# Performance work log

Hardware: AMD Instinct MI355X
Metric: run time of the kernel (lower is better)

## Reference

```python
import jax, jax.numpy as jnp
import numpy as np

D_MODEL = 256
NHEAD = 8
HEAD_DIM = D_MODEL // NHEAD
EPS = 1e-6
LN_EPS = 1e-5


def embed_rotary(x, cos, sin):
    # x, cos, sin: [N, L, C]; rotate even/odd pairs (Lepard-style RoFPE)
    x2 = jnp.stack([-x[..., 1::2], x[..., ::2]], axis=-1).reshape(x.shape)
    return x * cos + x2 * sin


def layer_norm(x, g, b):
    m = jnp.mean(x, axis=-1, keepdims=True)
    v = jnp.mean((x - m) ** 2, axis=-1, keepdims=True)
    return (x - m) / jnp.sqrt(v + LN_EPS) * g + b


def setup_inputs() -> dict:
    key = jax.random.key(0)
    ks = jax.random.split(key, 12)
    N, L, S, C = 8, 4096, 4096, D_MODEL
    s = 1.0 / np.sqrt(C)
    return {
        "x": jax.random.normal(ks[0], (N, L, C), jnp.float32),
        "source": jax.random.normal(ks[1], (N, S, C), jnp.float32),
        "x_pe": jax.random.normal(ks[2], (N, L, C, 2), jnp.float32),
        "source_pe": jax.random.normal(ks[3], (N, S, C, 2), jnp.float32),
        "Wq": jax.random.normal(ks[4], (C, C), jnp.float32) * s,
        "Wk": jax.random.normal(ks[5], (C, C), jnp.float32) * s,
        "Wv": jax.random.normal(ks[6], (C, C), jnp.float32) * s,
        "Wm": jax.random.normal(ks[7], (C, C), jnp.float32) * s,
        "W1": jax.random.normal(ks[8], (2 * C, 2 * C), jnp.float32) * s,
        "W2": jax.random.normal(ks[9], (2 * C, C), jnp.float32) * s,
        "ln1_g": jnp.ones((C,), jnp.float32),
        "ln1_b": jnp.zeros((C,), jnp.float32),
        "ln2_g": jnp.ones((C,), jnp.float32),
        "ln2_b": jnp.zeros((C,), jnp.float32),
    }


def reference(x, source, x_pe, source_pe, Wq, Wk, Wv, Wm, W1, W2, ln1_g, ln1_b, ln2_g, ln2_b):
    N, L, C = x.shape
    S = source.shape[1]
    H, D = NHEAD, HEAD_DIM

    query = x @ Wq           # [N, L, C]
    key = source @ Wk        # [N, S, C]
    value = source @ Wv      # [N, S, C]

    # ELU+1 feature maps (on pre-rotary projections)
    Q = jax.nn.elu(query) + 1.0
    K = jax.nn.elu(key) + 1.0

    q_cos, q_sin = x_pe[..., 0], x_pe[..., 1]
    k_cos, k_sin = source_pe[..., 0], source_pe[..., 1]
    Q_pos = embed_rotary(query, q_cos, q_sin)
    K_pos = embed_rotary(key, k_cos, k_sin)
    value = embed_rotary(value, k_cos, k_sin)

    Q = Q.reshape(N, L, H, D)
    K = K.reshape(N, S, H, D)
    Q_pos = Q_pos.reshape(N, L, H, D)
    K_pos = K_pos.reshape(N, S, H, D)
    value = value.reshape(N, S, H, D)

    values = value / S
    KV = jnp.einsum('nshd,nshv->nhdv', K_pos, values)          # [N, H, D, D]
    Z = 1.0 / (jnp.einsum('nlhd,nhd->nlh', Q, K.sum(axis=1)) + EPS)
    queried = jnp.einsum('nlhd,nhdv->nlhv', Q_pos, KV) * Z[..., None] * S  # [N, L, H, D]

    message = queried.reshape(N, L, C) @ Wm
    message = layer_norm(message, ln1_g, ln1_b)
    h = jnp.concatenate([x, message], axis=2) @ W1             # [N, L, 2C]
    h = jax.nn.relu(h)
    message = h @ W2                                            # [N, L, C]
    message = layer_norm(message, ln2_g, ln2_b)
    return x + message
```

## Files before the change

kernel.cpp:

```cpp
#include <hip/hip_runtime.h>

typedef __attribute__((ext_vector_type(8))) short bf16x8;
typedef __attribute__((ext_vector_type(4))) float f32x4;

__device__ __forceinline__ float bf2f(unsigned short b) {
    unsigned u = ((unsigned)b) << 16; float f;
    __builtin_memcpy(&f, &u, 4); return f;
}
__device__ __forceinline__ unsigned short f2bf(float f) {
    unsigned u; __builtin_memcpy(&u, &f, 4);
    unsigned r = u + 0x7FFFu + ((u >> 16) & 1u);
    return (unsigned short)(r >> 16);
}
__device__ __forceinline__ unsigned packbf(float a, float b) {
    return (unsigned)f2bf(a) | ((unsigned)f2bf(b) << 16);
}
__device__ __forceinline__ float elu1(float v) { return v > 0.f ? v + 1.f : __expf(v); }

__device__ __forceinline__ void async_copy16(const unsigned short* g, unsigned short* l) {
    __builtin_amdgcn_global_load_lds(
        (const __attribute__((address_space(1))) unsigned int*)g,
        (__attribute__((address_space(3))) unsigned int*)l, 16, 0, 0);
}

__device__ __host__ __forceinline__ int chan_of(int tc) {
    return (tc & ~63) | ((tc & 15) << 1) | ((tc >> 4) & 1) | (((tc >> 5) & 1) << 5);
}
__device__ __forceinline__ int chan_even(int gnb, int p, int low) {
    const int tc = gnb + 32 * p + low;
    return (tc & ~63) | ((tc & 15) << 1) | (((tc >> 5) & 1) << 5);
}

#define EPI_RELU 0
#define EPI_Q 1
#define EPI_KV 2
#define EPI_LN1 3
#define EPI_LN2RES 4

template <int MT, int NT, int EPI>
__global__ __launch_bounds__(256) void gemm_bt(
    const unsigned short* __restrict__ A, int lda,
    const unsigned short* __restrict__ B, int K,
    unsigned short* __restrict__ Cb, int ldc,
    const float* __restrict__ pe,
    const float* __restrict__ KsumC, float* __restrict__ KsumA,
    float* __restrict__ Zbuf, unsigned short* __restrict__ Qpos,
    unsigned short* __restrict__ KF, unsigned short* __restrict__ VF,
    const float* __restrict__ g, const float* __restrict__ bta,
    unsigned short* __restrict__ A2out,
    const float* __restrict__ xres, float* __restrict__ outF)
{
    constexpr int WM = MT / 2, WN = NT / 2, MI = WM / 16, NI = WN / 16;
    __shared__ unsigned short Asm[MT * 32];
    __shared__ unsigned short Bsm[NT * 32];
    const int t = threadIdx.x;
    const int lane = t & 63, w = t >> 6;
    const int wm = w & 1, wn = w >> 1;
    const int quad = lane >> 4, low = lane & 15;
    const int m0 = blockIdx.x * MT, n0 = blockIdx.y * NT;

    f32x4 acc[MI][NI];
#pragma unroll
    for (int i = 0; i < MI; i++)
#pragma unroll
        for (int j = 0; j < NI; j++) acc[i][j] = (f32x4){0.f, 0.f, 0.f, 0.f};

    for (int k0 = 0; k0 < K; k0 += 32) {
        __syncthreads();
#pragma unroll
        for (int i = 0; i < MT / 64; i++) {
            const int chunk = i * 256 + t;
            const int row = chunk >> 2, part = chunk & 3;
            async_copy16(A + (size_t)(m0 + row) * lda + k0 + part * 8,
                         Asm + (i * 256 + w * 64) * 8);
        }
#pragma unroll
        for (int i = 0; i < NT / 64; i++) {
            const int chunk = i * 256 + t;
            const int row = chunk >> 2, part = chunk & 3;
            async_copy16(B + (size_t)(n0 + row) * K + k0 + part * 8,
                         Bsm + (i * 256 + w * 64) * 8);
        }
        __syncthreads();
        bf16x8 a[MI], b[NI];
#pragma unroll
        for (int mi = 0; mi < MI; mi++)
            a[mi] = *(const bf16x8*)&Asm[(wm * WM + mi * 16 + low) * 32 + quad * 8];
#pragma unroll
        for (int ni = 0; ni < NI; ni++)
            b[ni] = *(const bf16x8*)&Bsm[(wn * WN + ni * 16 + low) * 32 + quad * 8];
#pragma unroll
        for (int mi = 0; mi < MI; mi++)
#pragma unroll
            for (int ni = 0; ni < NI; ni++)
                acc[mi][ni] = __builtin_amdgcn_mfma_f32_16x16x32_bf16(a[mi], b[ni], acc[mi][ni], 0, 0, 0);
    }

    const int gmb = m0 + wm * WM, gnb = n0 + wn * WN;

    if constexpr (EPI == EPI_RELU) {
#pragma unroll
        for (int mi = 0; mi < MI; mi++)
#pragma unroll
            for (int p = 0; p < NI / 2; p++) {
                const int c_e = chan_even(gnb, p, low);
#pragma unroll
                for (int r = 0; r < 4; r++) {
                    const int row = gmb + mi * 16 + quad * 4 + r;
                    const float ve = acc[mi][2 * p][r], vo = acc[mi][2 * p + 1][r];
                    *(unsigned*)&Cb[(size_t)row * ldc + c_e] =
                        packbf(ve > 0.f ? ve : 0.f, vo > 0.f ? vo : 0.f);
                }
            }
    } else if constexpr (EPI == EPI_Q) {
        const int n = m0 >> 12;
#pragma unroll
        for (int p = 0; p < NI / 2; p++) {
            const int c_e = chan_even(gnb, p, low);
            const int head = c_e >> 5;
            const float2 ks = *(const float2*)&KsumC[n * 256 + c_e];
#pragma unroll
            for (int mi = 0; mi < MI; mi++) {
#pragma unroll
                for (int r = 0; r < 4; r++) {
                    const int row = gmb + mi * 16 + quad * 4 + r;
                    const float4 cs = *(const float4*)&pe[((size_t)row * 256 + c_e) * 2];
                    const float ve = acc[mi][2 * p][r], vo = acc[mi][2 * p + 1][r];
                    *(unsigned*)&Qpos[(size_t)row * 256 + c_e] =
                        packbf(ve * cs.x - vo * cs.y, vo * cs.z + ve * cs.w);
                    float z = elu1(ve) * ks.x + elu1(vo) * ks.y;
                    z += __shfl_xor(z, 1); z += __shfl_xor(z, 2);
                    z += __shfl_xor(z, 4); z += __shfl_xor(z, 8);
                    if (low == 0) Zbuf[(size_t)row * 8 + head] = 1.f / (z + 1e-6f);
                }
            }
        }
    } else if constexpr (EPI == EPI_KV) {
        const int n = m0 >> 12;
#pragma unroll
        for (int p = 0; p < NI / 2; p++) {
            const int c_full = chan_even(gnb, p, low);
            const bool isK = c_full < 256;
            const int c = c_full & 255;
            const int nh = n * 8 + (c >> 5), d = c & 31;
            unsigned short* dst = isK ? KF : VF;
            float kel_e = 0.f, kel_o = 0.f;
#pragma unroll
            for (int mi = 0; mi < MI; mi++) {
                const int row0 = gmb + mi * 16 + quad * 4;
                const int s0 = row0 & 4095;
                unsigned short pk[8];
#pragma unroll
                for (int r = 0; r < 4; r++) {
                    const int row = row0 + r;
                    const float4 cs = *(const float4*)&pe[((size_t)row * 256 + c) * 2];
                    const float ve = acc[mi][2 * p][r], vo = acc[mi][2 * p + 1][r];
                    pk[r]     = f2bf(ve * cs.x - vo * cs.y);
                    pk[4 + r] = f2bf(vo * cs.z + ve * cs.w);
                    if (isK) { kel_e += elu1(ve); kel_o += elu1(vo); }
                }
                const size_t base = ((size_t)nh * 512 + (s0 >> 3)) * 32;
                *(uint2*)&dst[(base + d) * 8 + (s0 & 7)]     = *(const uint2*)&pk[0];
                *(uint2*)&dst[(base + d + 1) * 8 + (s0 & 7)] = *(const uint2*)&pk[4];
            }
            if (isK) {
                kel_e += __shfl_xor(kel_e, 16); kel_e += __shfl_xor(kel_e, 32);
                kel_o += __shfl_xor(kel_o, 16); kel_o += __shfl_xor(kel_o, 32);
                if (quad == 0) {
                    atomicAdd(&KsumA[n * 256 + c], kel_e);
                    atomicAdd(&KsumA[n * 256 + c + 1], kel_o);
                }
            }
        }
    } else {
        __shared__ float2 lnp[2][64];
        __syncthreads();
#pragma unroll
        for (int mi = 0; mi < MI; mi++)
#pragma unroll
            for (int r = 0; r < 4; r++) {
                float s1 = 0.f, s2 = 0.f;
#pragma unroll
                for (int ni = 0; ni < NI; ni++) {
                    const float v = acc[mi][ni][r];
                    s1 += v; s2 += v * v;
                }
                s1 += __shfl_xor(s1, 1); s2 += __shfl_xor(s2, 1);
                s1 += __shfl_xor(s1, 2); s2 += __shfl_xor(s2, 2);
                s1 += __shfl_xor(s1, 4); s2 += __shfl_xor(s2, 4);
                s1 += __shfl_xor(s1, 8); s2 += __shfl_xor(s2, 8);
                if (low == 0) lnp[wn][wm * WM + mi * 16 + quad * 4 + r] = make_float2(s1, s2);
            }
        __syncthreads();
#pragma unroll
        for (int mi = 0; mi < MI; mi++)
#pragma unroll
            for (int r = 0; r < 4; r++) {
                const int rl = wm * WM + mi * 16 + quad * 4 + r;
                const int row = m0 + rl;
                const float2 pa = lnp[0][rl], pb = lnp[1][rl];
                const float mean = (pa.x + pb.x) * (1.f / 256.f);
                const float var = (pa.y + pb.y) * (1.f / 256.f) - mean * mean;
                const float rstd = rsqrtf(var + 1e-5f);
#pragma unroll
                for (int p = 0; p < NI / 2; p++) {
                    const int c_e = chan_even(gnb, p, low);
                    const float2 gg = *(const float2*)&g[c_e];
                    const float2 bb = *(const float2*)&bta[c_e];
                    const float ve = acc[mi][2 * p][r], vo = acc[mi][2 * p + 1][r];
                    const float oe = (ve - mean) * rstd * gg.x + bb.x;
                    const float oo = (vo - mean) * rstd * gg.y + bb.y;
                    if constexpr (EPI == EPI_LN1) {
                        *(unsigned*)&A2out[(size_t)row * 512 + 256 + c_e] = packbf(oe, oo);
                    } else {
                        const float2 xv = *(const float2*)&xres[(size_t)row * 256 + c_e];
                        float2 o; o.x = xv.x + oe; o.y = xv.y + oo;
                        *(float2*)&outF[(size_t)row * 256 + c_e] = o;
                    }
                }
            }
    }
}

__global__ void prep_weights(const float* __restrict__ Wq, const float* __restrict__ Wk,
                             const float* __restrict__ Wv, const float* __restrict__ Wm,
                             const float* __restrict__ W1, const float* __restrict__ W2,
                             unsigned short* __restrict__ WqT, unsigned short* __restrict__ WkvT,
                             unsigned short* __restrict__ WmT, unsigned short* __restrict__ W1T,
                             unsigned short* __restrict__ W2T, float* __restrict__ zero_base) {
    const int idx = blockIdx.x * 256 + threadIdx.x;
    if (idx < 65536) {
        const int tc = idx >> 8, k = idx & 255;
        WqT[idx] = f2bf(Wq[(size_t)k * 256 + chan_of(tc)]);
    } else if (idx < 196608) {
        const int i = idx - 65536, tc = i >> 8, k = i & 255;
        const int c = chan_of(tc);
        WkvT[i] = f2bf(c < 256 ? Wk[(size_t)k * 256 + c] : Wv[(size_t)k * 256 + (c - 256)]);
    } else if (idx < 262144) {
        const int i = idx - 196608, tc = i >> 8, k = i & 255;
        WmT[i] = f2bf(Wm[(size_t)k * 256 + chan_of(tc)]);
    } else if (idx < 524288) {
        const int i = idx - 262144, tc = i >> 9, k = i & 511;
        W1T[i] = f2bf(W1[(size_t)k * 512 + chan_of(tc)]);
    } else if (idx < 655360) {
        const int i = idx - 524288, tc = i >> 9, k = i & 511;
        W2T[i] = f2bf(W2[(size_t)k * 256 + chan_of(tc)]);
    } else {
        zero_base[idx - 655360] = 0.f;
    }
}

__global__ void conv_bf16(const float* __restrict__ src, unsigned short* __restrict__ dst, int dstride) {
    const int idx = blockIdx.x * 256 + threadIdx.x;
    const int row = idx >> 6;
    const int c0 = (idx & 63) * 4;
    const float4 v = *(const float4*)&src[(size_t)row * 256 + c0];
    unsigned short o[4] = {f2bf(v.x), f2bf(v.y), f2bf(v.z), f2bf(v.w)};
    *(uint2*)&dst[(size_t)row * dstride + c0] = *(const uint2*)o;
}

__global__ __launch_bounds__(256) void kv2_kernel(const unsigned short* __restrict__ KF,
                                                  const unsigned short* __restrict__ VF,
                                                  float* __restrict__ KVT) {
    const int nh = blockIdx.x, sc = blockIdx.y;
    const int t = threadIdx.x, lane = t & 63, w = t >> 6;
    const int quad = lane >> 4, low = lane & 15;
    const int sbase = sc * 1024 + w * 256;

    f32x4 acc[2][2];
#pragma unroll
    for (int i = 0; i < 2; i++)
#pragma unroll
        for (int j = 0; j < 2; j++) acc[i][j] = (f32x4){0.f, 0.f, 0.f, 0.f};

    for (int s0 = 0; s0 < 256; s0 += 32) {
        const int sk = sbase + s0 + quad * 8;
        const size_t cb = ((size_t)nh * 512 + (sk >> 3)) * 32;
        bf16x8 a[2], b[2];
#pragma unroll
        for (int mi = 0; mi < 2; mi++)
            a[mi] = *(const bf16x8*)&KF[(cb + mi * 16 + low) * 8];
#pragma unroll
        for (int ni = 0; ni < 2; ni++)
            b[ni] = *(const bf16x8*)&VF[(cb + ni * 16 + low) * 8];
#pragma unroll
        for (int mi = 0; mi < 2; mi++)
#pragma unroll
            for (int ni = 0; ni < 2; ni++)
                acc[mi][ni] = __builtin_amdgcn_mfma_f32_16x16x32_bf16(a[mi], b[ni], acc[mi][ni], 0, 0, 0);
    }

    __shared__ float red[4][1024];
#pragma unroll
    for (int mi = 0; mi < 2; mi++)
#pragma unroll
        for (int ni = 0; ni < 2; ni++)
#pragma unroll
            for (int r = 0; r < 4; r++)
                red[w][(mi * 16 + quad * 4 + r) * 32 + ni * 16 + low] = acc[mi][ni][r];
    __syncthreads();
#pragma unroll
    for (int k = 0; k < 4; k++) {
        const int i = t + k * 256;
        const float s = red[0][i] + red[1][i] + red[2][i] + red[3][i];
        atomicAdd(&KVT[(size_t)nh * 1024 + (size_t)(i & 31) * 32 + (i >> 5)], s);
    }
}

__global__ __launch_bounds__(256) void attn_out_kernel(const unsigned short* __restrict__ Qpos,
                                                       const float* __restrict__ KVT,
                                                       const float* __restrict__ Zbuf,
                                                       unsigned short* __restrict__ Qrd) {
    const int h = blockIdx.y, mt = blockIdx.x;
    const int t = threadIdx.x, lane = t & 63, w = t >> 6;
    const int quad = lane >> 4, low = lane & 15;
    const int rbase = mt * 256 + w * 64;
    const int n = rbase >> 12;

    bf16x8 b[2];
#pragma unroll
    for (int ni = 0; ni < 2; ni++) {
        const float* src = &KVT[((size_t)(n * 8 + h) * 32 + ni * 16 + low) * 32 + quad * 8];
        short tmp[8];
#pragma unroll
        for (int j = 0; j < 8; j++) tmp[j] = (short)f2bf(src[j]);
        __builtin_memcpy(&b[ni], tmp, 16);
    }

    f32x4 acc[4][2];
#pragma unroll
    for (int i = 0; i < 4; i++)
#pragma unroll
        for (int j = 0; j < 2; j++) acc[i][j] = (f32x4){0.f, 0.f, 0.f, 0.f};

#pragma unroll
    for (int mi = 0; mi < 4; mi++) {
        const bf16x8 a = *(const bf16x8*)&Qpos[((size_t)(rbase + mi * 16 + low)) * 256 + h * 32 + quad * 8];
#pragma unroll
        for (int ni = 0; ni < 2; ni++)
            acc[mi][ni] = __builtin_amdgcn_mfma_f32_16x16x32_bf16(a, b[ni], acc[mi][ni], 0, 0, 0);
    }

#pragma unroll
    for (int mi = 0; mi < 4; mi++)
#pragma unroll
        for (int ni = 0; ni < 2; ni++)
#pragma unroll
            for (int r = 0; r < 4; r++) {
                const int row = rbase + mi * 16 + quad * 4 + r;
                const int col = h * 32 + ni * 16 + low;
                Qrd[(size_t)row * 256 + col] = f2bf(acc[mi][ni][r] * Zbuf[(size_t)row * 8 + h]);
            }
}

extern "C" void kernel_launch(void* const* d_in, const int* in_sizes, int n_in,
                              void* d_out, int out_size, void* d_ws, size_t ws_size,
                              hipStream_t stream) {
    const float* x   = (const float*)d_in[0];
    const float* src = (const float*)d_in[1];
    const float* xpe = (const float*)d_in[2];
    const float* spe = (const float*)d_in[3];
    const float* Wq  = (const float*)d_in[4];
    const float* Wk  = (const float*)d_in[5];
    const float* Wv  = (const float*)d_in[6];
    const float* Wm  = (const float*)d_in[7];
    const float* W1  = (const float*)d_in[8];
    const float* W2  = (const float*)d_in[9];
    const float* g1  = (const float*)d_in[10];
    const float* b1  = (const float*)d_in[11];
    const float* g2  = (const float*)d_in[12];
    const float* b2  = (const float*)d_in[13];

    char* p = (char*)d_ws;
    unsigned short* WqT  = (unsigned short*)p; p += 256 * 256 * 2;
    unsigned short* WkvT = (unsigned short*)p; p += 512 * 256 * 2;
    unsigned short* WmT  = (unsigned short*)p; p += 256 * 256 * 2;
    unsigned short* W1T  = (unsigned short*)p; p += 512 * 512 * 2;
    unsigned short* W2T  = (unsigned short*)p; p += 256 * 512 * 2;
    float* KVT  = (float*)p; p += 64 * 1024 * 4;
    float* Ksum = (float*)p; p += 8 * 256 * 4;
    float* Zbuf = (float*)p; p += (size_t)32768 * 8 * 4;
    unsigned short* A2   = (unsigned short*)p; p += (size_t)32768 * 512 * 2;
    unsigned short* srcB = (unsigned short*)p; p += (size_t)32768 * 256 * 2;
    unsigned short* KF   = (unsigned short*)p; p += (size_t)32768 * 256 * 2;
    unsigned short* VF   = (unsigned short*)p; p += (size_t)32768 * 256 * 2;
    unsigned short* Qpos = (unsigned short*)p; p += (size_t)32768 * 256 * 2;
    unsigned short* Qrd  = (unsigned short*)p; p += (size_t)32768 * 256 * 2;
    unsigned short* hbuf = KF;

    prep_weights<<<2824, 256, 0, stream>>>(Wq, Wk, Wv, Wm, W1, W2,
                                           WqT, WkvT, WmT, W1T, W2T, KVT);
    conv_bf16<<<8192, 256, 0, stream>>>(x, A2, 512);
    conv_bf16<<<8192, 256, 0, stream>>>(src, srcB, 256);

    gemm_bt<128, 128, EPI_KV><<<dim3(256, 4), 256, 0, stream>>>(
        srcB, 256, WkvT, 256, nullptr, 0, spe, nullptr, Ksum,
        nullptr, nullptr, KF, VF, nullptr, nullptr, nullptr, nullptr, nullptr);
    kv2_kernel<<<dim3(64, 4), 256, 0, stream>>>(KF, VF, KVT);

    gemm_bt<128, 128, EPI_Q><<<dim3(256, 2), 256, 0, stream>>>(
        A2, 512, WqT, 256, nullptr, 0, xpe, Ksum, nullptr,
        Zbuf, Qpos, nullptr, nullptr, nullptr, nullptr, nullptr, nullptr, nullptr);

    attn_out_kernel<<<dim3(128, 8), 256, 0, stream>>>(Qpos, KVT, Zbuf, Qrd);

    gemm_bt<64, 256, EPI_LN1><<<512, 256, 0, stream>>>(
        Qrd, 256, WmT, 256, nullptr, 0, nullptr, nullptr, nullptr,
        nullptr, nullptr, nullptr, nullptr, g1, b1, A2, nullptr, nullptr);

    gemm_bt<128, 128, EPI_RELU><<<dim3(256, 4), 256, 0, stream>>>(
        A2, 512, W1T, 512, hbuf, 512, nullptr, nullptr, nullptr,
        nullptr, nullptr, nullptr, nullptr, nullptr, nullptr, nullptr, nullptr, nullptr);

    gemm_bt<64, 256, EPI_LN2RES><<<512, 256, 0, stream>>>(
        hbuf, 512, W2T, 512, nullptr, 0, nullptr, nullptr, nullptr,
        nullptr, nullptr, nullptr, nullptr, g2, b2, nullptr, x, (float*)d_out);
}
```

Before: 402.9 us.

## Double-buffer GEMM LDS tiles with XOR swizzle and retile to 64x256

The GEMM main loop now uses two LDS buffers. The next k-slice is prefetched asynchronously while the current one feeds the MFMAs, so there is one barrier per step instead of two. The LDS chunk order is XOR-swizzled to cut bank conflicts on the bf16x8 reads. The KV, Q and ReLU GEMMs switch to 64x256 tiles, and the K/V weight channel interleave changes so each 256-wide tile covers matching K and V channels. Launch bounds request 4 blocks per CU. The doubled LDS footprint and the register cap could limit occupancy or cause spills.

```diff
diff --git a/kernel.cpp b/kernel.cpp
--- a/kernel.cpp
+++ b/kernel.cpp
@@ -38,7 +38,7 @@
 #define EPI_LN2RES 4
 
 template <int MT, int NT, int EPI>
-__global__ __launch_bounds__(256) void gemm_bt(
+__global__ __launch_bounds__(256, 4) void gemm_bt(
     const unsigned short* __restrict__ A, int lda,
     const unsigned short* __restrict__ B, int K,
     unsigned short* __restrict__ Cb, int ldc,
@@ -51,8 +51,8 @@
     const float* __restrict__ xres, float* __restrict__ outF)
 {
     constexpr int WM = MT / 2, WN = NT / 2, MI = WM / 16, NI = WN / 16;
-    __shared__ unsigned short Asm[MT * 32];
-    __shared__ unsigned short Bsm[NT * 32];
+    __shared__ unsigned short Asm[2][MT * 32];
+    __shared__ unsigned short Bsm[2][NT * 32];
     const int t = threadIdx.x;
     const int lane = t & 63, w = t >> 6;
     const int wm = w & 1, wn = w >> 1;
@@ -65,30 +65,41 @@
 #pragma unroll
         for (int j = 0; j < NI; j++) acc[i][j] = (f32x4){0.f, 0.f, 0.f, 0.f};
 
-    for (int k0 = 0; k0 < K; k0 += 32) {
-        __syncthreads();
+    auto stage = [&](int k0, int buf) {
 #pragma unroll
         for (int i = 0; i < MT / 64; i++) {
             const int chunk = i * 256 + t;
-            const int row = chunk >> 2, part = chunk & 3;
+            const int row = chunk >> 2;
+            const int part = (chunk & 3) ^ ((chunk >> 3) & 3);
             async_copy16(A + (size_t)(m0 + row) * lda + k0 + part * 8,
-                         Asm + (i * 256 + w * 64) * 8);
+                         &Asm[buf][(i * 256 + w * 64) * 8]);
         }
 #pragma unroll
         for (int i = 0; i < NT / 64; i++) {
             const int chunk = i * 256 + t;
-            const int row = chunk >> 2, part = chunk & 3;
+            const int row = chunk >> 2;
+            const int part = (chunk & 3) ^ ((chunk >> 3) & 3);
             async_copy16(B + (size_t)(n0 + row) * K + k0 + part * 8,
-                         Bsm + (i * 256 + w * 64) * 8);
+                         &Bsm[buf][(i * 256 + w * 64) * 8]);
         }
-        __syncthreads();
+    };
+
+    const int nk = K >> 5;
+    const int swz = (low >> 1) & 3;
+    stage(0, 0);
+    int kb = 0;
+    for (int ks = 0; ks < nk; ks++, kb ^= 1) {
+        asm volatile("s_waitcnt vmcnt(0)" ::: "memory");
+        __builtin_amdgcn_s_barrier();
+        __builtin_amdgcn_sched_barrier(0);
+        if (ks + 1 < nk) stage((ks + 1) << 5, kb ^ 1);
         bf16x8 a[MI], b[NI];
 #pragma unroll
         for (int mi = 0; mi < MI; mi++)
-            a[mi] = *(const bf16x8*)&Asm[(wm * WM + mi * 16 + low) * 32 + quad * 8];
+            a[mi] = *(const bf16x8*)&Asm[kb][(wm * WM + mi * 16 + low) * 32 + ((quad ^ swz)) * 8];
 #pragma unroll
         for (int ni = 0; ni < NI; ni++)
-            b[ni] = *(const bf16x8*)&Bsm[(wn * WN + ni * 16 + low) * 32 + quad * 8];
+            b[ni] = *(const bf16x8*)&Bsm[kb][(wn * WN + ni * 16 + low) * 32 + ((quad ^ swz)) * 8];
 #pragma unroll
         for (int mi = 0; mi < MI; mi++)
 #pragma unroll
@@ -139,9 +150,9 @@
         const int n = m0 >> 12;
 #pragma unroll
         for (int p = 0; p < NI / 2; p++) {
-            const int c_full = chan_even(gnb, p, low);
-            const bool isK = c_full < 256;
-            const int c = c_full & 255;
+            const int tcg = gnb + 32 * p;
+            const bool isK = ((tcg >> 5) & 1) == 0;
+            const int c = ((tcg & ~63) >> 1) | (low << 1);
             const int nh = n * 8 + (c >> 5), d = c & 31;
             unsigned short* dst = isK ? KF : VF;
             float kel_e = 0.f, kel_o = 0.f;
@@ -234,8 +245,9 @@
         WqT[idx] = f2bf(Wq[(size_t)k * 256 + chan_of(tc)]);
     } else if (idx < 196608) {
         const int i = idx - 65536, tc = i >> 8, k = i & 255;
-        const int c = chan_of(tc);
-        WkvT[i] = f2bf(c < 256 ? Wk[(size_t)k * 256 + c] : Wv[(size_t)k * 256 + (c - 256)]);
+        const int f = (tc >> 5) & 1;
+        const int c = ((tc & ~63) >> 1) | ((tc & 15) << 1) | ((tc >> 4) & 1);
+        WkvT[i] = f2bf(f ? Wv[(size_t)k * 256 + c] : Wk[(size_t)k * 256 + c]);
     } else if (idx < 262144) {
         const int i = idx - 196608, tc = i >> 8, k = i & 255;
         WmT[i] = f2bf(Wm[(size_t)k * 256 + chan_of(tc)]);
@@ -393,12 +405,12 @@
     conv_bf16<<<8192, 256, 0, stream>>>(x, A2, 512);
     conv_bf16<<<8192, 256, 0, stream>>>(src, srcB, 256);
 
-    gemm_bt<128, 128, EPI_KV><<<dim3(256, 4), 256, 0, stream>>>(
+    gemm_bt<64, 256, EPI_KV><<<dim3(512, 2), 256, 0, stream>>>(
         srcB, 256, WkvT, 256, nullptr, 0, spe, nullptr, Ksum,
         nullptr, nullptr, KF, VF, nullptr, nullptr, nullptr, nullptr, nullptr);
     kv2_kernel<<<dim3(64, 4), 256, 0, stream>>>(KF, VF, KVT);
 
-    gemm_bt<128, 128, EPI_Q><<<dim3(256, 2), 256, 0, stream>>>(
+    gemm_bt<64, 256, EPI_Q><<<dim3(512, 1), 256, 0, stream>>>(
         A2, 512, WqT, 256, nullptr, 0, xpe, Ksum, nullptr,
         Zbuf, Qpos, nullptr, nullptr, nullptr, nullptr, nullptr, nullptr, nullptr);
 
@@ -408,7 +420,7 @@
         Qrd, 256, WmT, 256, nullptr, 0, nullptr, nullptr, nullptr,
         nullptr, nullptr, nullptr, nullptr, g1, b1, A2, nullptr, nullptr);
 
-    gemm_bt<128, 128, EPI_RELU><<<dim3(256, 4), 256, 0, stream>>>(
+    gemm_bt<64, 256, EPI_RELU><<<dim3(512, 2), 256, 0, stream>>>(
         A2, 512, W1T, 512, hbuf, 512, nullptr, nullptr, nullptr,
         nullptr, nullptr, nullptr, nullptr, nullptr, nullptr, nullptr, nullptr, nullptr);
 
```

Result: faster. 391.9 us (-2.7%).
